# Performance work log

Measured on AMD Instinct MI355X. Metric: run time of the kernel, lower is better.

The kernel has to match this reference:

```python
import jax, jax.numpy as jnp
import numpy as np

K = 2  # forward hardcodes k = 2, overriding the k_vector argmax


def setup_inputs() -> dict:
    key = jax.random.key(0)
    k1, k2, k3 = jax.random.split(key, 3)
    points = jax.random.uniform(k1, (4, 8000, 3), dtype=jnp.float32)
    preds = jax.random.uniform(k2, (4, 8000, 256), dtype=jnp.float32)
    k_vector = jax.random.normal(k3, (2,), dtype=jnp.float32)
    return {"points": points, "preds": preds, "k_vector": k_vector}


def reference(points, preds, k_vector):
    # k = argmax(softmax(k_vector)) + 1 is computed then discarded; k = 2.
    # Pairwise euclidean distance (torch.cdist, p=2): [B, N, N]
    sq = jnp.sum(points * points, axis=-1)  # [B, N]
    d2 = sq[:, :, None] + sq[:, None, :] - 2.0 * jnp.einsum(
        'bnd,bmd->bnm', points, points)
    dist = jnp.sqrt(jnp.maximum(d2, 0.0))
    # k smallest distances -> indices of K nearest neighbors (incl. self)
    _, idx = jax.lax.top_k(-dist, K)  # idx: [B, N, K]
    # Gather neighbor features and average: [B, N, K, C] -> [B, N, C]
    knn_preds = jax.vmap(lambda p, i: p[i])(preds, idx)
    return jnp.mean(knn_preds, axis=2)
```

## Files before the change

### kernel.cpp

```cpp
#include <hip/hip_runtime.h>
#include <math.h>

#define BATCH 4
#define NPTS  8000
#define NCH   256
#define GDIM  20
#define NCELL (GDIM*GDIM*GDIM)
#define CELLH (1.0f/GDIM)
#define EPS   1e-5f

#define STRIDE_ST (NCELL + 16)
#define WS_STARTS 0
#define WS_PSORT  131072

__device__ __forceinline__ int cell_clamp(float v) {
  int c = (int)(v * (float)GDIM);
  return c < 0 ? 0 : (c > GDIM - 1 ? GDIM - 1 : c);
}

__global__ __launch_bounds__(1024) void build_kernel(const float* __restrict__ points,
                                                     int* __restrict__ starts,
                                                     float4* __restrict__ psort) {
  __shared__ int lst[NCELL];
  __shared__ int wtot[16];
  const int t = threadIdx.x;
  const int b = blockIdx.x;
  if (t < 1000) {
#pragma unroll
    for (int k = 0; k < 8; ++k) lst[t * 8 + k] = 0;
  }
  __syncthreads();

  const float* pb = points + (size_t)b * NPTS * 3;
  float px[8], py[8], pz[8];
  int pc[8];
#pragma unroll
  for (int k = 0; k < 8; ++k) {
    const int j = t + k * 1024;
    pc[k] = -1;
    if (j < NPTS) {
      px[k] = pb[j * 3 + 0];
      py[k] = pb[j * 3 + 1];
      pz[k] = pb[j * 3 + 2];
      pc[k] = (cell_clamp(pz[k]) * GDIM + cell_clamp(py[k])) * GDIM + cell_clamp(px[k]);
      atomicAdd(&lst[pc[k]], 1);
    }
  }
  __syncthreads();

  int v[8];
  int sum = 0;
  if (t < 1000) {
#pragma unroll
    for (int k = 0; k < 8; ++k) {
      v[k] = lst[t * 8 + k];
      sum += v[k];
    }
  }
  const int lane = t & 63, wv = t >> 6;
  int incl = sum;
#pragma unroll
  for (int d = 1; d < 64; d <<= 1) {
    const int u = __shfl_up(incl, d);
    if (lane >= d) incl += u;
  }
  if (lane == 63) wtot[wv] = incl;
  __syncthreads();
  if (wv == 0) {
    int x = (lane < 16) ? wtot[lane] : 0;
#pragma unroll
    for (int d = 1; d < 16; d <<= 1) {
      const int u = __shfl_up(x, d);
      if (lane >= d) x += u;
    }
    if (lane < 16) wtot[lane] = x;
  }
  __syncthreads();
  const int base = incl - sum + (wv ? wtot[wv - 1] : 0);

  int* stg = starts + b * STRIDE_ST;
  if (t < 1000) {
    int run = base;
#pragma unroll
    for (int k = 0; k < 8; ++k) {
      stg[t * 8 + k] = run;
      lst[t * 8 + k] = run;
      run += v[k];
    }
  }
  if (t == 0) stg[NCELL] = NPTS;
  __syncthreads();

  float4* psb = psort + (size_t)b * NPTS;
#pragma unroll
  for (int k = 0; k < 8; ++k) {
    if (pc[k] >= 0) {
      const int pos = atomicAdd(&lst[pc[k]], 1);
      psb[pos] = make_float4(px[k], py[k], pz[k], __int_as_float(t + k * 1024));
    }
  }
}

#define SCAN_RANGE(P0, P1)                                        \
  for (int p = (P0); p < (P1); ++p) {                             \
    const float4 P = ps[p];                                       \
    const float dot = xi * P.x + yi * P.y + zi * P.z;             \
    const float sqj = P.x * P.x + P.y * P.y + P.z * P.z;          \
    const float d2 = fmaxf((sqi + sqj) - 2.0f * dot, 0.0f);       \
    const int j = __float_as_int(P.w);                            \
    const bool lt = (p != i) &&                                   \
        ((d2 < b0) || (d2 == b0 && j < j0));                      \
    b0 = lt ? d2 : b0;                                            \
    j0 = lt ? j : j0;                                             \
  }

#define MERGE_XOR(MASK)                                           \
  {                                                               \
    const float ob = __shfl_xor(mb0, MASK);                       \
    const int oj = __shfl_xor(mj0, MASK);                         \
    const bool keep = (mb0 < ob) || (mb0 == ob && mj0 < oj);      \
    mb0 = keep ? mb0 : ob;                                        \
    mj0 = keep ? mj0 : oj;                                        \
  }

__global__ __launch_bounds__(256, 8) void search_gather_kernel(
    const float4* __restrict__ psort, const int* __restrict__ starts,
    const float* __restrict__ preds, float* __restrict__ out) {
  __shared__ int snbr[16][2];
  const int t = threadIdx.x;
  const int b = blockIdx.y;
  const int* stg = starts + b * STRIDE_ST;

  const int ql = t >> 4;
  const int s = t & 15;
  const int i = blockIdx.x * 16 + ql;
  const float4* ps = psort + (size_t)b * NPTS;
  const float4 Q = ps[i];
  const float xi = Q.x, yi = Q.y, zi = Q.z;
  const int qorig = __float_as_int(Q.w);
  const float sqi = xi * xi + yi * yi + zi * zi;
  const int cx = cell_clamp(xi), cy = cell_clamp(yi), cz = cell_clamp(zi);
  const int x0c = cx > 1 ? cx - 2 : 0;
  const int x1c = cx < GDIM - 2 ? cx + 2 : GDIM - 1;

  float b0 = INFINITY;
  int j0 = -1;

  int rs[2], re[2];
#pragma unroll
  for (int rr = 0; rr < 2; ++rr) {
    const int kk = s + rr * 16;
    int lo = 0, hi = 0;
    if (kk < 25) {
      const int z = cz + kk / 5 - 2;
      const int y = cy + kk % 5 - 2;
      if ((unsigned)z < GDIM && (unsigned)y < GDIM) {
        const int rowbase = (z * GDIM + y) * GDIM;
        lo = stg[rowbase + x0c];
        hi = stg[rowbase + x1c + 1];
      }
    }
    rs[rr] = lo;
    re[rr] = hi;
  }
#pragma unroll
  for (int rr = 0; rr < 2; ++rr) { SCAN_RANGE(rs[rr], re[rr]) }

  float mb0 = b0;
  int mj0 = j0;
  MERGE_XOR(1) MERGE_XOR(2) MERGE_XOR(4) MERGE_XOR(8)

  if (!(mb0 + EPS <= (2.0f * CELLH) * (2.0f * CELLH))) {
    for (int r = 3; r <= GDIM; ++r) {
      const int W = 2 * r + 1;
      for (int idx = s; idx < W * W; idx += 16) {
        const int dz = idx / W - r;
        const int dy = idx % W - r;
        const int z = cz + dz, y = cy + dy;
        if ((unsigned)z >= GDIM || (unsigned)y >= GDIM) continue;
        const int rowbase = (z * GDIM + y) * GDIM;
        if (dz == -r || dz == r || dy == -r || dy == r) {
          const int xl = cx > r ? cx - r : 0;
          const int xh = cx < GDIM - 1 - r ? cx + r : GDIM - 1;
          const int lo = stg[rowbase + xl], hi = stg[rowbase + xh + 1];
          SCAN_RANGE(lo, hi)
        } else {
          if (cx - r >= 0) {
            const int lo = stg[rowbase + cx - r], hi = stg[rowbase + cx - r + 1];
            SCAN_RANGE(lo, hi)
          }
          if (cx + r <= GDIM - 1) {
            const int lo = stg[rowbase + cx + r], hi = stg[rowbase + cx + r + 1];
            SCAN_RANGE(lo, hi)
          }
        }
      }
      mb0 = b0; mj0 = j0;
      MERGE_XOR(1) MERGE_XOR(2) MERGE_XOR(4) MERGE_XOR(8)
      const float rb = (float)r * CELLH;
      if (mb0 + EPS <= rb * rb) break;
    }
  }

  if (s == 0) {
    snbr[ql][0] = mj0;
    snbr[ql][1] = qorig;
  }
  __syncthreads();

  const int wave = t >> 6;
  const int lane = t & 63;
  const float* predb = preds + (size_t)b * NPTS * NCH;
  float* outb = out + (size_t)b * NPTS * NCH;
#pragma unroll
  for (int k = 0; k < 4; ++k) {
    const int q = wave * 4 + k;
    const int c = snbr[q][0];
    const int qo = snbr[q][1];
    const float4 va = ((const float4*)(predb + (size_t)qo * NCH))[lane];
    const float4 vc = ((const float4*)(predb + (size_t)c * NCH))[lane];
    float4 r;
    r.x = 0.5f * (va.x + vc.x);
    r.y = 0.5f * (va.y + vc.y);
    r.z = 0.5f * (va.z + vc.z);
    r.w = 0.5f * (va.w + vc.w);
    ((float4*)(outb + (size_t)qo * NCH))[lane] = r;
  }
}

extern "C" void kernel_launch(void* const* d_in, const int* in_sizes, int n_in,
                              void* d_out, int out_size, void* d_ws, size_t ws_size,
                              hipStream_t stream) {
  const float* points = (const float*)d_in[0];
  const float* preds = (const float*)d_in[1];
  float* out = (float*)d_out;

  char* ws = (char*)d_ws;
  int* starts = (int*)(ws + WS_STARTS);
  float4* psort = (float4*)(ws + WS_PSORT);

  build_kernel<<<BATCH, 1024, 0, stream>>>(points, starts, psort);
  search_gather_kernel<<<dim3(NPTS / 16, BATCH), 256, 0, stream>>>(psort, starts, preds, out);
}
```

Before: 35.58 us.

## Assign one wave per query, scanning 125 single cells across lanes

Each query is now handled by a full 64-lane wave instead of 16 threads. The 5x5x5 neighbourhood is split into 125 individual cells, two per lane, instead of 25 x-rows, which shrinks each lane's serial scan. The query's own feature row is loaded early so it overlaps the search, and the shared-memory neighbour handoff and block barrier are gone. The cost is four times as many blocks, two extra shuffle-merge steps, and more per-lane cell-start lookups.

```diff
diff --git a/kernel.cpp b/kernel.cpp
--- a/kernel.cpp
+++ b/kernel.cpp
@@ -126,54 +126,61 @@
 __global__ __launch_bounds__(256, 8) void search_gather_kernel(
     const float4* __restrict__ psort, const int* __restrict__ starts,
     const float* __restrict__ preds, float* __restrict__ out) {
-  __shared__ int snbr[16][2];
   const int t = threadIdx.x;
   const int b = blockIdx.y;
+  const int wv = t >> 6;
+  const int lane = t & 63;
+  const int i = blockIdx.x * 4 + wv;
   const int* stg = starts + b * STRIDE_ST;
-
-  const int ql = t >> 4;
-  const int s = t & 15;
-  const int i = blockIdx.x * 16 + ql;
   const float4* ps = psort + (size_t)b * NPTS;
+
   const float4 Q = ps[i];
   const float xi = Q.x, yi = Q.y, zi = Q.z;
   const int qorig = __float_as_int(Q.w);
   const float sqi = xi * xi + yi * yi + zi * zi;
+
+  const float* predb = preds + (size_t)b * NPTS * NCH;
+  const float4 va = ((const float4*)(predb + (size_t)qorig * NCH))[lane];
+
   const int cx = cell_clamp(xi), cy = cell_clamp(yi), cz = cell_clamp(zi);
-  const int x0c = cx > 1 ? cx - 2 : 0;
-  const int x1c = cx < GDIM - 2 ? cx + 2 : GDIM - 1;
+
+  int lo0 = 0, hi0 = 0, lo1 = 0, hi1 = 0;
+  {
+    const int c = lane;
+    const int dz = c / 25 - 2;
+    const int rem = c % 25;
+    const int z = cz + dz, y = cy + rem / 5 - 2, x = cx + rem % 5 - 2;
+    if ((unsigned)z < GDIM && (unsigned)y < GDIM && (unsigned)x < GDIM) {
+      const int cid = (z * GDIM + y) * GDIM + x;
+      lo0 = stg[cid];
+      hi0 = stg[cid + 1];
+    }
+  }
+  if (lane < 61) {
+    const int c = lane + 64;
+    const int dz = c / 25 - 2;
+    const int rem = c % 25;
+    const int z = cz + dz, y = cy + rem / 5 - 2, x = cx + rem % 5 - 2;
+    if ((unsigned)z < GDIM && (unsigned)y < GDIM && (unsigned)x < GDIM) {
+      const int cid = (z * GDIM + y) * GDIM + x;
+      lo1 = stg[cid];
+      hi1 = stg[cid + 1];
+    }
+  }
 
   float b0 = INFINITY;
   int j0 = -1;
-
-  int rs[2], re[2];
-#pragma unroll
-  for (int rr = 0; rr < 2; ++rr) {
-    const int kk = s + rr * 16;
-    int lo = 0, hi = 0;
-    if (kk < 25) {
-      const int z = cz + kk / 5 - 2;
-      const int y = cy + kk % 5 - 2;
-      if ((unsigned)z < GDIM && (unsigned)y < GDIM) {
-        const int rowbase = (z * GDIM + y) * GDIM;
-        lo = stg[rowbase + x0c];
-        hi = stg[rowbase + x1c + 1];
-      }
-    }
-    rs[rr] = lo;
-    re[rr] = hi;
-  }
-#pragma unroll
-  for (int rr = 0; rr < 2; ++rr) { SCAN_RANGE(rs[rr], re[rr]) }
+  SCAN_RANGE(lo0, hi0)
+  SCAN_RANGE(lo1, hi1)
 
   float mb0 = b0;
   int mj0 = j0;
-  MERGE_XOR(1) MERGE_XOR(2) MERGE_XOR(4) MERGE_XOR(8)
+  MERGE_XOR(1) MERGE_XOR(2) MERGE_XOR(4) MERGE_XOR(8) MERGE_XOR(16) MERGE_XOR(32)
 
   if (!(mb0 + EPS <= (2.0f * CELLH) * (2.0f * CELLH))) {
     for (int r = 3; r <= GDIM; ++r) {
       const int W = 2 * r + 1;
-      for (int idx = s; idx < W * W; idx += 16) {
+      for (int idx = lane; idx < W * W; idx += 64) {
         const int dz = idx / W - r;
         const int dy = idx % W - r;
         const int z = cz + dz, y = cy + dy;
@@ -196,36 +203,20 @@
         }
       }
       mb0 = b0; mj0 = j0;
-      MERGE_XOR(1) MERGE_XOR(2) MERGE_XOR(4) MERGE_XOR(8)
+      MERGE_XOR(1) MERGE_XOR(2) MERGE_XOR(4) MERGE_XOR(8) MERGE_XOR(16) MERGE_XOR(32)
       const float rb = (float)r * CELLH;
       if (mb0 + EPS <= rb * rb) break;
     }
   }
 
-  if (s == 0) {
-    snbr[ql][0] = mj0;
-    snbr[ql][1] = qorig;
-  }
-  __syncthreads();
-
-  const int wave = t >> 6;
-  const int lane = t & 63;
-  const float* predb = preds + (size_t)b * NPTS * NCH;
+  const float4 vc = ((const float4*)(predb + (size_t)mj0 * NCH))[lane];
+  float4 r;
+  r.x = 0.5f * (va.x + vc.x);
+  r.y = 0.5f * (va.y + vc.y);
+  r.z = 0.5f * (va.z + vc.z);
+  r.w = 0.5f * (va.w + vc.w);
   float* outb = out + (size_t)b * NPTS * NCH;
-#pragma unroll
-  for (int k = 0; k < 4; ++k) {
-    const int q = wave * 4 + k;
-    const int c = snbr[q][0];
-    const int qo = snbr[q][1];
-    const float4 va = ((const float4*)(predb + (size_t)qo * NCH))[lane];
-    const float4 vc = ((const float4*)(predb + (size_t)c * NCH))[lane];
-    float4 r;
-    r.x = 0.5f * (va.x + vc.x);
-    r.y = 0.5f * (va.y + vc.y);
-    r.z = 0.5f * (va.z + vc.z);
-    r.w = 0.5f * (va.w + vc.w);
-    ((float4*)(outb + (size_t)qo * NCH))[lane] = r;
-  }
+  ((float4*)(outb + (size_t)qorig * NCH))[lane] = r;
 }
 
 extern "C" void kernel_launch(void* const* d_in, const int* in_sizes, int n_in,
@@ -240,5 +231,5 @@
   float4* psort = (float4*)(ws + WS_PSORT);
 
   build_kernel<<<BATCH, 1024, 0, stream>>>(points, starts, psort);
-  search_gather_kernel<<<dim3(NPTS / 16, BATCH), 256, 0, stream>>>(psort, starts, preds, out);
-}
+  search_gather_kernel<<<dim3(NPTS / 4, BATCH), 256, 0, stream>>>(psort, starts, preds, out);
+}
```

Result: slower. 39.35 us (+10.6%).

## Search 3x3x3 neighborhood first, vectorize point loads, replace LDS handoff with shuffles

Applied to the files above, without the earlier changes.

The nearest-neighbor search now first scans only the 27 adjacent cells and stops early if the best distance is within one cell width. Only if that test fails does it fall back to the previous 5x5 row scan and then the expanding shells. This cuts the number of candidate points scanned per query for the typical density. The build kernel loads points as contiguous float4 vectors per thread, renumbering original indices as t*8+k. The gather step takes neighbor indices through wave shuffles instead of shared memory plus __syncthreads.

```diff
diff --git a/kernel.cpp b/kernel.cpp
--- a/kernel.cpp
+++ b/kernel.cpp
@@ -34,14 +34,20 @@
   const float* pb = points + (size_t)b * NPTS * 3;
   float px[8], py[8], pz[8];
   int pc[8];
-#pragma unroll
-  for (int k = 0; k < 8; ++k) {
-    const int j = t + k * 1024;
-    pc[k] = -1;
-    if (j < NPTS) {
-      px[k] = pb[j * 3 + 0];
-      py[k] = pb[j * 3 + 1];
-      pz[k] = pb[j * 3 + 2];
+  if (t < 1000) {
+    const float4* pv = (const float4*)pb;
+    const float4 a0 = pv[t * 6 + 0], a1 = pv[t * 6 + 1], a2 = pv[t * 6 + 2];
+    const float4 a3 = pv[t * 6 + 3], a4 = pv[t * 6 + 4], a5 = pv[t * 6 + 5];
+    px[0] = a0.x; py[0] = a0.y; pz[0] = a0.z;
+    px[1] = a0.w; py[1] = a1.x; pz[1] = a1.y;
+    px[2] = a1.z; py[2] = a1.w; pz[2] = a2.x;
+    px[3] = a2.y; py[3] = a2.z; pz[3] = a2.w;
+    px[4] = a3.x; py[4] = a3.y; pz[4] = a3.z;
+    px[5] = a3.w; py[5] = a4.x; pz[5] = a4.y;
+    px[6] = a4.z; py[6] = a4.w; pz[6] = a5.x;
+    px[7] = a5.y; py[7] = a5.z; pz[7] = a5.w;
+#pragma unroll
+    for (int k = 0; k < 8; ++k) {
       pc[k] = (cell_clamp(pz[k]) * GDIM + cell_clamp(py[k])) * GDIM + cell_clamp(px[k]);
       atomicAdd(&lst[pc[k]], 1);
     }
@@ -92,11 +98,11 @@
   __syncthreads();
 
   float4* psb = psort + (size_t)b * NPTS;
-#pragma unroll
-  for (int k = 0; k < 8; ++k) {
-    if (pc[k] >= 0) {
+  if (t < 1000) {
+#pragma unroll
+    for (int k = 0; k < 8; ++k) {
       const int pos = atomicAdd(&lst[pc[k]], 1);
-      psb[pos] = make_float4(px[k], py[k], pz[k], __int_as_float(t + k * 1024));
+      psb[pos] = make_float4(px[k], py[k], pz[k], __int_as_float(t * 8 + k));
     }
   }
 }
@@ -126,97 +132,120 @@
 __global__ __launch_bounds__(256, 8) void search_gather_kernel(
     const float4* __restrict__ psort, const int* __restrict__ starts,
     const float* __restrict__ preds, float* __restrict__ out) {
-  __shared__ int snbr[16][2];
   const int t = threadIdx.x;
   const int b = blockIdx.y;
-  const int* stg = starts + b * STRIDE_ST;
-
   const int ql = t >> 4;
   const int s = t & 15;
   const int i = blockIdx.x * 16 + ql;
+  const int* stg = starts + b * STRIDE_ST;
   const float4* ps = psort + (size_t)b * NPTS;
   const float4 Q = ps[i];
   const float xi = Q.x, yi = Q.y, zi = Q.z;
   const int qorig = __float_as_int(Q.w);
   const float sqi = xi * xi + yi * yi + zi * zi;
   const int cx = cell_clamp(xi), cy = cell_clamp(yi), cz = cell_clamp(zi);
-  const int x0c = cx > 1 ? cx - 2 : 0;
-  const int x1c = cx < GDIM - 2 ? cx + 2 : GDIM - 1;
 
   float b0 = INFINITY;
   int j0 = -1;
 
-  int rs[2], re[2];
-#pragma unroll
-  for (int rr = 0; rr < 2; ++rr) {
-    const int kk = s + rr * 16;
-    int lo = 0, hi = 0;
-    if (kk < 25) {
-      const int z = cz + kk / 5 - 2;
-      const int y = cy + kk % 5 - 2;
-      if ((unsigned)z < GDIM && (unsigned)y < GDIM) {
-        const int rowbase = (z * GDIM + y) * GDIM;
-        lo = stg[rowbase + x0c];
-        hi = stg[rowbase + x1c + 1];
-      }
-    }
-    rs[rr] = lo;
-    re[rr] = hi;
-  }
-#pragma unroll
-  for (int rr = 0; rr < 2; ++rr) { SCAN_RANGE(rs[rr], re[rr]) }
+  {
+    int lo0 = 0, hi0 = 0, lo1 = 0, hi1 = 0;
+    {
+      const int c = s;
+      const int dz = c / 9 - 1;
+      const int rem = c % 9;
+      const int z = cz + dz, y = cy + rem / 3 - 1, x = cx + rem % 3 - 1;
+      if ((unsigned)z < GDIM && (unsigned)y < GDIM && (unsigned)x < GDIM) {
+        const int cid = (z * GDIM + y) * GDIM + x;
+        lo0 = stg[cid];
+        hi0 = stg[cid + 1];
+      }
+    }
+    if (s < 11) {
+      const int c = s + 16;
+      const int dz = c / 9 - 1;
+      const int rem = c % 9;
+      const int z = cz + dz, y = cy + rem / 3 - 1, x = cx + rem % 3 - 1;
+      if ((unsigned)z < GDIM && (unsigned)y < GDIM && (unsigned)x < GDIM) {
+        const int cid = (z * GDIM + y) * GDIM + x;
+        lo1 = stg[cid];
+        hi1 = stg[cid + 1];
+      }
+    }
+    SCAN_RANGE(lo0, hi0)
+    SCAN_RANGE(lo1, hi1)
+  }
 
   float mb0 = b0;
   int mj0 = j0;
   MERGE_XOR(1) MERGE_XOR(2) MERGE_XOR(4) MERGE_XOR(8)
 
-  if (!(mb0 + EPS <= (2.0f * CELLH) * (2.0f * CELLH))) {
-    for (int r = 3; r <= GDIM; ++r) {
-      const int W = 2 * r + 1;
-      for (int idx = s; idx < W * W; idx += 16) {
-        const int dz = idx / W - r;
-        const int dy = idx % W - r;
-        const int z = cz + dz, y = cy + dy;
-        if ((unsigned)z >= GDIM || (unsigned)y >= GDIM) continue;
-        const int rowbase = (z * GDIM + y) * GDIM;
-        if (dz == -r || dz == r || dy == -r || dy == r) {
-          const int xl = cx > r ? cx - r : 0;
-          const int xh = cx < GDIM - 1 - r ? cx + r : GDIM - 1;
-          const int lo = stg[rowbase + xl], hi = stg[rowbase + xh + 1];
-          SCAN_RANGE(lo, hi)
-        } else {
-          if (cx - r >= 0) {
-            const int lo = stg[rowbase + cx - r], hi = stg[rowbase + cx - r + 1];
+  if (!(mb0 + EPS <= CELLH * CELLH)) {
+    const int x0c = cx > 1 ? cx - 2 : 0;
+    const int x1c = cx < GDIM - 2 ? cx + 2 : GDIM - 1;
+    int rs[2], re[2];
+#pragma unroll
+    for (int rr = 0; rr < 2; ++rr) {
+      const int kk = s + rr * 16;
+      int lo = 0, hi = 0;
+      if (kk < 25) {
+        const int z = cz + kk / 5 - 2;
+        const int y = cy + kk % 5 - 2;
+        if ((unsigned)z < GDIM && (unsigned)y < GDIM) {
+          const int rowbase = (z * GDIM + y) * GDIM;
+          lo = stg[rowbase + x0c];
+          hi = stg[rowbase + x1c + 1];
+        }
+      }
+      rs[rr] = lo;
+      re[rr] = hi;
+    }
+#pragma unroll
+    for (int rr = 0; rr < 2; ++rr) { SCAN_RANGE(rs[rr], re[rr]) }
+
+    mb0 = b0; mj0 = j0;
+    MERGE_XOR(1) MERGE_XOR(2) MERGE_XOR(4) MERGE_XOR(8)
+
+    if (!(mb0 + EPS <= (2.0f * CELLH) * (2.0f * CELLH))) {
+      for (int r = 3; r <= GDIM; ++r) {
+        const int W = 2 * r + 1;
+        for (int idx = s; idx < W * W; idx += 16) {
+          const int dz = idx / W - r;
+          const int dy = idx % W - r;
+          const int z = cz + dz, y = cy + dy;
+          if ((unsigned)z >= GDIM || (unsigned)y >= GDIM) continue;
+          const int rowbase = (z * GDIM + y) * GDIM;
+          if (dz == -r || dz == r || dy == -r || dy == r) {
+            const int xl = cx > r ? cx - r : 0;
+            const int xh = cx < GDIM - 1 - r ? cx + r : GDIM - 1;
+            const int lo = stg[rowbase + xl], hi = stg[rowbase + xh + 1];
             SCAN_RANGE(lo, hi)
-          }
-          if (cx + r <= GDIM - 1) {
-            const int lo = stg[rowbase + cx + r], hi = stg[rowbase + cx + r + 1];
-            SCAN_RANGE(lo, hi)
+          } else {
+            if (cx - r >= 0) {
+              const int lo = stg[rowbase + cx - r], hi = stg[rowbase + cx - r + 1];
+              SCAN_RANGE(lo, hi)
+            }
+            if (cx + r <= GDIM - 1) {
+              const int lo = stg[rowbase + cx + r], hi = stg[rowbase + cx + r + 1];
+              SCAN_RANGE(lo, hi)
+            }
           }
         }
-      }
-      mb0 = b0; mj0 = j0;
-      MERGE_XOR(1) MERGE_XOR(2) MERGE_XOR(4) MERGE_XOR(8)
-      const float rb = (float)r * CELLH;
-      if (mb0 + EPS <= rb * rb) break;
-    }
-  }
-
-  if (s == 0) {
-    snbr[ql][0] = mj0;
-    snbr[ql][1] = qorig;
-  }
-  __syncthreads();
-
-  const int wave = t >> 6;
+        mb0 = b0; mj0 = j0;
+        MERGE_XOR(1) MERGE_XOR(2) MERGE_XOR(4) MERGE_XOR(8)
+        const float rb = (float)r * CELLH;
+        if (mb0 + EPS <= rb * rb) break;
+      }
+    }
+  }
+
   const int lane = t & 63;
   const float* predb = preds + (size_t)b * NPTS * NCH;
   float* outb = out + (size_t)b * NPTS * NCH;
 #pragma unroll
   for (int k = 0; k < 4; ++k) {
-    const int q = wave * 4 + k;
-    const int c = snbr[q][0];
-    const int qo = snbr[q][1];
+    const int c = __shfl(mj0, k * 16);
+    const int qo = __shfl(qorig, k * 16);
     const float4 va = ((const float4*)(predb + (size_t)qo * NCH))[lane];
     const float4 vc = ((const float4*)(predb + (size_t)c * NCH))[lane];
     float4 r;
```

Result: faster. 34.58 us (-2.8%).
